# Kernel optimization log

Hardware: AMD Instinct MI355X
Metric: run time of the kernel (lower is better)

Reference implementation:

```python
import jax, jax.numpy as jnp
import numpy as np

N_LIG, N_TGT, E = 100000, 4000, 150000
D_LIG, D_TGT, H = 4, 1280, 128


def _seg_mean(feat, idx, n):
    # segment mean; isolated nodes get 0 (PyG mean aggr semantics)
    s = jax.ops.segment_sum(feat, idx, num_segments=n)
    c = jax.ops.segment_sum(jnp.ones((idx.shape[0], 1), feat.dtype), idx, num_segments=n)
    return s / jnp.maximum(c, 1.0)


def setup_inputs() -> dict:
    key = jax.random.key(0)
    ks = jax.random.split(key, 20)
    s = 0.05  # weight scale
    inp = {
        'x_ligand': jax.random.normal(ks[0], (N_LIG, D_LIG), jnp.float32),
        'x_target': jax.random.normal(ks[1], (N_TGT, D_TGT), jnp.float32),
        'edge_index': jnp.stack([
            jax.random.randint(ks[2], (E,), 0, N_LIG, jnp.int32),
            jax.random.randint(ks[3], (E,), 0, N_TGT, jnp.int32),
        ]),
        'W1lt_l': jax.random.normal(ks[4], (D_LIG, H), jnp.float32) * s,
        'b1lt':   jax.random.normal(ks[5], (H,), jnp.float32) * s,
        'W1lt_r': jax.random.normal(ks[6], (D_TGT, H), jnp.float32) * s,
        'W1tl_l': jax.random.normal(ks[7], (D_TGT, H), jnp.float32) * s,
        'b1tl':   jax.random.normal(ks[8], (H,), jnp.float32) * s,
        'W1tl_r': jax.random.normal(ks[9], (D_LIG, H), jnp.float32) * s,
        'W2lt_l': jax.random.normal(ks[10], (H, H), jnp.float32) * s,
        'b2lt':   jax.random.normal(ks[11], (H,), jnp.float32) * s,
        'W2lt_r': jax.random.normal(ks[12], (H, H), jnp.float32) * s,
        'W2tl_l': jax.random.normal(ks[13], (H, H), jnp.float32) * s,
        'b2tl':   jax.random.normal(ks[14], (H,), jnp.float32) * s,
        'W2tl_r': jax.random.normal(ks[15], (H, H), jnp.float32) * s,
        'Wp':     jax.random.normal(ks[16], (2 * H, 1), jnp.float32) * s,
        'bp':     jax.random.normal(ks[17], (1,), jnp.float32) * s,
    }
    return inp


def reference(x_ligand, x_target, edge_index,
              W1lt_l, b1lt, W1lt_r, W1tl_l, b1tl, W1tl_r,
              W2lt_l, b2lt, W2lt_r, W2tl_l, b2tl, W2tl_r, Wp, bp):
    src, dst = edge_index[0], edge_index[1]  # ligand idx, target idx

    # conv1: SAGEConv  out = lin_l(mean_j x_src[j]) + lin_r(x_dst)
    m_t = _seg_mean(x_ligand[src], dst, N_TGT)              # [N_TGT, D_LIG]
    h_t = m_t @ W1lt_l + b1lt + x_target @ W1lt_r           # [N_TGT, H]
    m_l = _seg_mean(x_target[dst], src, N_LIG)              # [N_LIG, D_TGT]
    h_l = m_l @ W1tl_l + b1tl + x_ligand @ W1tl_r           # [N_LIG, H]
    h_t = jax.nn.relu(h_t)
    h_l = jax.nn.relu(h_l)

    # conv2 (hidden -> hidden), same edge structure
    m_t2 = _seg_mean(h_l[src], dst, N_TGT)
    h_t2 = jax.nn.relu(m_t2 @ W2lt_l + b2lt + h_t @ W2lt_r)
    m_l2 = _seg_mean(h_t[dst], src, N_LIG)
    h_l2 = jax.nn.relu(m_l2 @ W2tl_l + b2tl + h_l @ W2tl_r)

    # edge predictor: gather-cat-linear
    edge_feats = jnp.concatenate([h_l2[src], h_t2[dst]], axis=-1)  # [E, 2H]
    out = (edge_feats @ Wp + bp).squeeze(-1)                        # [E]
    return out
```

## Files before the change

### kernel.cpp

```cpp
#include <hip/hip_runtime.h>
#include <hip/hip_bf16.h>

#define N_LIG 100000
#define N_TGT 4000
#define NEDGE 150000
#define DT 1280
#define HD 128
#define CAP_L 32
#define CAP_T 128
#define NTILE_L 6250
#define NTILE_PAD 6252
#define PL_BLOCKS 1563

typedef __attribute__((ext_vector_type(8))) short short8v;
typedef __attribute__((ext_vector_type(4))) float f32x4;

static __device__ __forceinline__ ushort f2bf(float f) {
    __hip_bfloat16 h = __float2bfloat16(f);
    union { __hip_bfloat16 h; ushort u; } c; c.h = h; return c.u;
}
static __device__ __forceinline__ float bf2f(ushort u) {
    union { unsigned v; float f; } c; c.v = ((unsigned)u) << 16; return c.f;
}

__global__ __launch_bounds__(256) void k_pack(
    const float* __restrict__ W2, uint4* __restrict__ Wf,
    const float* __restrict__ Wr, const float* __restrict__ Wl,
    uint4* __restrict__ Wf1,
    const float* __restrict__ xt, uint4* __restrict__ xtf,
    int4* __restrict__ cntz,
    const float* __restrict__ W2a, const float* __restrict__ W2b,
    uint4* __restrict__ Wf2)
{
    int bx = blockIdx.x;
    if (bx < 8) {
        int gid = bx * 256 + threadIdx.x;
        int lane = gid & 63, frag = gid >> 6;
        int ks = frag >> 3, ct = frag & 7;
        int l15 = lane & 15, g = lane >> 4;
        int k = ks * 32 + g * 4, n = ct * 16 + l15;
        union { ushort us[8]; uint4 u; } o;
#pragma unroll
        for (int j = 0; j < 4; ++j) {
            o.us[j]     = f2bf(W2[(size_t)(k + j) * HD + n]);
            o.us[4 + j] = f2bf(W2[(size_t)(k + 16 + j) * HD + n]);
        }
        Wf[gid] = o.u;
    } else if (bx < 168) {
        int gid = (bx - 8) * 256 + threadIdx.x;
        int lane = gid & 63, frag = gid >> 6;
        int ks = frag >> 4, nct = frag & 15;
        int l15 = lane & 15, g = lane >> 4;
        int k = ks * 32 + g * 4, n = nct * 16 + l15;
        const float* Ws = (n < HD) ? Wr : Wl;
        int nn = n & 127;
        union { ushort us[8]; uint4 u; } o;
#pragma unroll
        for (int j = 0; j < 4; ++j) {
            o.us[j]     = f2bf(Ws[(size_t)(k + j) * HD + nn]);
            o.us[4 + j] = f2bf(Ws[(size_t)(k + 16 + j) * HD + nn]);
        }
        Wf1[gid] = o.u;
    } else if (bx < 2668) {
        int gid = (bx - 168) * 256 + threadIdx.x;
        int lane = gid & 63, frag = gid >> 6;
        int ks = frag % 40, rt = frag / 40;
        int row = rt * 16 + (lane & 15);
        int kb = ks * 32 + (lane >> 4) * 4;
        float4 a0 = *reinterpret_cast<const float4*>(xt + (size_t)row * DT + kb);
        float4 a1 = *reinterpret_cast<const float4*>(xt + (size_t)row * DT + kb + 16);
        union { ushort us[8]; uint4 u; } o;
        o.us[0] = f2bf(a0.x); o.us[1] = f2bf(a0.y); o.us[2] = f2bf(a0.z); o.us[3] = f2bf(a0.w);
        o.us[4] = f2bf(a1.x); o.us[5] = f2bf(a1.y); o.us[6] = f2bf(a1.z); o.us[7] = f2bf(a1.w);
        xtf[gid] = o.u;
    } else if (bx < 2770) {
        int i = (bx - 2668) * 256 + threadIdx.x;
        if (i < 26000) cntz[i] = make_int4(0, 0, 0, 0);
    } else {
        int gid = (bx - 2770) * 256 + threadIdx.x;
        int lane = gid & 63, frag = gid >> 6;
        int ks = frag >> 4, nct = frag & 15;
        int l15 = lane & 15, g = lane >> 4;
        int k = ks * 32 + g * 4, n = nct * 16 + l15;
        const float* Ws = (n < HD) ? W2a : W2b;
        int nn = n & 127;
        union { ushort us[8]; uint4 u; } o;
#pragma unroll
        for (int j = 0; j < 4; ++j) {
            o.us[j]     = f2bf(Ws[(size_t)(k + j) * HD + nn]);
            o.us[4 + j] = f2bf(Ws[(size_t)(k + 16 + j) * HD + nn]);
        }
        Wf2[gid] = o.u;
    }
}

__global__ __launch_bounds__(256) void k_fill(
    const int* __restrict__ src, const int* __restrict__ dst,
    int* __restrict__ cnt_src, int* __restrict__ cnt_dst,
    int* __restrict__ bsrc, int* __restrict__ bdst)
{
    int e = blockIdx.x * 256 + threadIdx.x;
    if (e >= NEDGE) return;
    int s = src[e], d = dst[e];
    int ps = atomicAdd(&cnt_src[s], 1);
    if (ps < CAP_L) bsrc[(size_t)s * CAP_L + ps] = d;
    int pd = atomicAdd(&cnt_dst[d], 1);
    if (pd < CAP_T) bdst[(size_t)d * CAP_T + pd] = s;
}

__global__ __launch_bounds__(512) void k_tgt1m(
    const uint4* __restrict__ xtf,
    const uint4* __restrict__ Wf1,
    const uint4* __restrict__ Wf2,
    const float* __restrict__ xl,
    const int* __restrict__ bdst, const int* __restrict__ cnt_dst,
    const float* __restrict__ W1lt_l,
    const float* __restrict__ b1lt,
    float* __restrict__ y_t1,
    float* __restrict__ y_t2, float* __restrict__ htW2r)
{
    __shared__ float  ms[16][4];
    __shared__ ushort hts[16][136];

    int w = threadIdx.x >> 6;
    int lane = threadIdx.x & 63;
    int l15 = lane & 15, g = lane >> 4;
    int rt = blockIdx.x;
    int row0 = rt * 16;

    if (threadIdx.x < 128) {
        int r = threadIdx.x >> 3, lane8 = threadIdx.x & 7;
        int row = row0 + r;
        int deg = cnt_dst[row];
        int n = min(deg, CAP_T);
        float4 acc = make_float4(0.f, 0.f, 0.f, 0.f);
        for (int i = lane8; i < n; i += 8) {
            int sid = bdst[(size_t)row * CAP_T + i];
            float4 x = *reinterpret_cast<const float4*>(xl + 4ull * (unsigned)sid);
            acc.x += x.x; acc.y += x.y; acc.z += x.z; acc.w += x.w;
        }
#pragma unroll
        for (int off = 1; off < 8; off <<= 1) {
            acc.x += __shfl_xor(acc.x, off); acc.y += __shfl_xor(acc.y, off);
            acc.z += __shfl_xor(acc.z, off); acc.w += __shfl_xor(acc.w, off);
        }
        if (lane8 == 0) {
            float dinv = 1.0f / fmaxf((float)deg, 1.0f);
            ms[r][0] = acc.x * dinv; ms[r][1] = acc.y * dinv;
            ms[r][2] = acc.z * dinv; ms[r][3] = acc.w * dinv;
        }
    }

    f32x4 acc[2];
#pragma unroll
    for (int ct = 0; ct < 2; ++ct) acc[ct] = (f32x4){0.f, 0.f, 0.f, 0.f};

    for (int ks = 0; ks < DT / 32; ++ks) {
        union { uint4 u; short8v s; } ua;
        ua.u = xtf[(size_t)(rt * 40 + ks) * 64 + lane];
#pragma unroll
        for (int ct = 0; ct < 2; ++ct) {
            union { uint4 u; short8v s; } ub;
            ub.u = Wf1[(size_t)(ks * 16 + w * 2 + ct) * 64 + lane];
            acc[ct] = __builtin_amdgcn_mfma_f32_16x16x32_bf16(ua.s, ub.s, acc[ct], 0, 0, 0);
        }
    }

    __syncthreads();

    if (w < 4) {
#pragma unroll
        for (int ct = 0; ct < 2; ++ct) {
            int c = w * 32 + ct * 16 + l15;
            float wl0 = W1lt_l[c], wl1 = W1lt_l[HD + c],
                  wl2 = W1lt_l[2 * HD + c], wl3 = W1lt_l[3 * HD + c];
            float bb = b1lt[c];
#pragma unroll
            for (int j = 0; j < 4; ++j) {
                int r = 4 * g + j;
                float v = acc[ct][j] + bb + ms[r][0] * wl0 + ms[r][1] * wl1
                        + ms[r][2] * wl2 + ms[r][3] * wl3;
                hts[r][c] = f2bf(fmaxf(v, 0.0f));
            }
        }
    } else {
#pragma unroll
        for (int ct = 0; ct < 2; ++ct) {
            int c = (w - 4) * 32 + ct * 16 + l15;
#pragma unroll
            for (int j = 0; j < 4; ++j) {
                int grow = row0 + 4 * g + j;
                y_t1[(size_t)grow * HD + c] = acc[ct][j];
            }
        }
    }
    __syncthreads();

    f32x4 acc2[2];
#pragma unroll
    for (int ct = 0; ct < 2; ++ct) acc2[ct] = (f32x4){0.f, 0.f, 0.f, 0.f};

#pragma unroll
    for (int ks2 = 0; ks2 < 4; ++ks2) {
        int kb2 = ks2 * 32 + g * 4;
        union { ushort us[8]; short8v s; } ua2;
        *reinterpret_cast<ushort4*>(&ua2.us[0]) =
            *reinterpret_cast<const ushort4*>(&hts[l15][kb2]);
        *reinterpret_cast<ushort4*>(&ua2.us[4]) =
            *reinterpret_cast<const ushort4*>(&hts[l15][kb2 + 16]);
#pragma unroll
        for (int ct = 0; ct < 2; ++ct) {
            union { uint4 u; short8v s; } ub2;
            ub2.u = Wf2[(size_t)(ks2 * 16 + w * 2 + ct) * 64 + lane];
            acc2[ct] = __builtin_amdgcn_mfma_f32_16x16x32_bf16(ua2.s, ub2.s, acc2[ct], 0, 0, 0);
        }
    }

    float* outp = (w < 4) ? y_t2 : htW2r;
    int cw = (w < 4) ? w : (w - 4);
#pragma unroll
    for (int ct = 0; ct < 2; ++ct) {
        int c = cw * 32 + ct * 16 + l15;
#pragma unroll
        for (int j = 0; j < 4; ++j) {
            int grow = row0 + 4 * g + j;
            outp[(size_t)grow * HD + c] = acc2[ct][j];
        }
    }
}

__global__ __launch_bounds__(256) void k_hl(
    const float* __restrict__ xl,
    const float* __restrict__ y_t1, const float* __restrict__ y_t2,
    const int* __restrict__ bsrc, const int* __restrict__ cnt_src,
    const float* __restrict__ W1tl_r,
    const float* __restrict__ b1tl,
    ushort* __restrict__ hlb, uint4* __restrict__ hlbf,
    ushort* __restrict__ gl2)
{
    int tc = threadIdx.x & 15;
    int node = blockIdx.x * 16 + (threadIdx.x >> 4);
    int ks = tc >> 2, g = tc & 3;
    int kb = ks * 32 + g * 4;

    int deg = cnt_src[node];
    int n = min(deg, CAP_L);
    float4 s0 = make_float4(0.f, 0.f, 0.f, 0.f);
    float4 s1 = make_float4(0.f, 0.f, 0.f, 0.f);
    float4 t0 = make_float4(0.f, 0.f, 0.f, 0.f);
    float4 t1 = make_float4(0.f, 0.f, 0.f, 0.f);
    for (int i = 0; i < n; ++i) {
        int did = bsrc[(size_t)node * CAP_L + i];
        float4 v0 = *reinterpret_cast<const float4*>(y_t1 + (size_t)did * HD + kb);
        float4 v1 = *reinterpret_cast<const float4*>(y_t1 + (size_t)did * HD + kb + 16);
        float4 u0 = *reinterpret_cast<const float4*>(y_t2 + (size_t)did * HD + kb);
        float4 u1 = *reinterpret_cast<const float4*>(y_t2 + (size_t)did * HD + kb + 16);
        s0.x += v0.x; s0.y += v0.y; s0.z += v0.z; s0.w += v0.w;
        s1.x += v1.x; s1.y += v1.y; s1.z += v1.z; s1.w += v1.w;
        t0.x += u0.x; t0.y += u0.y; t0.z += u0.z; t0.w += u0.w;
        t1.x += u1.x; t1.y += u1.y; t1.z += u1.z; t1.w += u1.w;
    }
    float dinv = 1.0f / fmaxf((float)deg, 1.0f);
    float4 x = *reinterpret_cast<const float4*>(xl + 4ull * (unsigned)node);

    float4 b0 = *reinterpret_cast<const float4*>(b1tl + kb);
    float4 b1 = *reinterpret_cast<const float4*>(b1tl + kb + 16);
    float4 wa0 = *reinterpret_cast<const float4*>(W1tl_r + 0 * HD + kb);
    float4 wa1 = *reinterpret_cast<const float4*>(W1tl_r + 1 * HD + kb);
    float4 wa2 = *reinterpret_cast<const float4*>(W1tl_r + 2 * HD + kb);
    float4 wa3 = *reinterpret_cast<const float4*>(W1tl_r + 3 * HD + kb);
    float4 wb0 = *reinterpret_cast<const float4*>(W1tl_r + 0 * HD + kb + 16);
    float4 wb1 = *reinterpret_cast<const float4*>(W1tl_r + 1 * HD + kb + 16);
    float4 wb2 = *reinterpret_cast<const float4*>(W1tl_r + 2 * HD + kb + 16);
    float4 wb3 = *reinterpret_cast<const float4*>(W1tl_r + 3 * HD + kb + 16);

    union { ushort us[8]; uint4 u; ushort4 h[2]; } o;
    o.us[0] = f2bf(fmaxf(s0.x * dinv + b0.x + x.x * wa0.x + x.y * wa1.x + x.z * wa2.x + x.w * wa3.x, 0.f));
    o.us[1] = f2bf(fmaxf(s0.y * dinv + b0.y + x.x * wa0.y + x.y * wa1.y + x.z * wa2.y + x.w * wa3.y, 0.f));
    o.us[2] = f2bf(fmaxf(s0.z * dinv + b0.z + x.x * wa0.z + x.y * wa1.z + x.z * wa2.z + x.w * wa3.z, 0.f));
    o.us[3] = f2bf(fmaxf(s0.w * dinv + b0.w + x.x * wa0.w + x.y * wa1.w + x.z * wa2.w + x.w * wa3.w, 0.f));
    o.us[4] = f2bf(fmaxf(s1.x * dinv + b1.x + x.x * wb0.x + x.y * wb1.x + x.z * wb2.x + x.w * wb3.x, 0.f));
    o.us[5] = f2bf(fmaxf(s1.y * dinv + b1.y + x.x * wb0.y + x.y * wb1.y + x.z * wb2.y + x.w * wb3.y, 0.f));
    o.us[6] = f2bf(fmaxf(s1.z * dinv + b1.z + x.x * wb0.z + x.y * wb1.z + x.z * wb2.z + x.w * wb3.z, 0.f));
    o.us[7] = f2bf(fmaxf(s1.w * dinv + b1.w + x.x * wb0.w + x.y * wb1.w + x.z * wb2.w + x.w * wb3.w, 0.f));

    *reinterpret_cast<ushort4*>(hlb + (size_t)node * HD + kb)      = o.h[0];
    *reinterpret_cast<ushort4*>(hlb + (size_t)node * HD + kb + 16) = o.h[1];
    int lane = (node & 15) + 16 * g;
    hlbf[(size_t)(blockIdx.x * 4 + ks) * 64 + lane] = o.u;

    ushort4 q0, q1;
    q0.x = f2bf(t0.x * dinv); q0.y = f2bf(t0.y * dinv);
    q0.z = f2bf(t0.z * dinv); q0.w = f2bf(t0.w * dinv);
    q1.x = f2bf(t1.x * dinv); q1.y = f2bf(t1.y * dinv);
    q1.z = f2bf(t1.z * dinv); q1.w = f2bf(t1.w * dinv);
    *reinterpret_cast<ushort4*>(gl2 + (size_t)node * HD + kb)      = q0;
    *reinterpret_cast<ushort4*>(gl2 + (size_t)node * HD + kb + 16) = q1;
}

__global__ __launch_bounds__(256) void k_ptl(
    const ushort* __restrict__ hlb,
    const uint4* __restrict__ hlbf,
    const uint4* __restrict__ Wf,
    const ushort* __restrict__ gl2,
    const int* __restrict__ bdst, const int* __restrict__ cnt_dst,
    const float* __restrict__ Wlt,
    const float* __restrict__ b2lt,
    const float* __restrict__ b2tl,
    const float* __restrict__ htW2r,
    const float* __restrict__ Wp,
    float* __restrict__ p_t, float* __restrict__ p_l)
{
    __shared__ int   idx[CAP_T];
    __shared__ float sm[16][132];
    __shared__ float msh[HD];
    __shared__ float sum2[2];

    if (blockIdx.x < N_TGT) {
        int row = blockIdx.x;
        int deg = cnt_dst[row];
        int nn = min(deg, CAP_T);

        if (threadIdx.x < CAP_T) idx[threadIdx.x] = bdst[(size_t)row * CAP_T + threadIdx.x];
        __syncthreads();

        int wg = threadIdx.x >> 4, l16 = threadIdx.x & 15;
        float s[8];
#pragma unroll
        for (int j = 0; j < 8; ++j) s[j] = 0.f;
        for (int i = wg; i < nn; i += 16) {
            int sid = idx[i];
            union { uint4 u; ushort us[8]; } v;
            v.u = *reinterpret_cast<const uint4*>(hlb + (size_t)sid * HD + l16 * 8);
#pragma unroll
            for (int j = 0; j < 8; ++j) s[j] += bf2f(v.us[j]);
        }
#pragma unroll
        for (int j = 0; j < 8; ++j) sm[wg][l16 * 8 + j] = s[j];
        __syncthreads();

        if (threadIdx.x < HD) {
            int h = threadIdx.x;
            float dinv = 1.0f / fmaxf((float)deg, 1.0f);
            float acc = 0.f;
#pragma unroll
            for (int w2 = 0; w2 < 16; ++w2) acc += sm[w2][h];
            msh[h] = acc * dinv;
        }
        __syncthreads();

        if (threadIdx.x < HD) {
            int h = threadIdx.x;
            float g = 0.f;
            for (int k = 0; k < HD; k += 4) {
                float4 mk = *reinterpret_cast<const float4*>(&msh[k]);
                g += mk.x * Wlt[(size_t)(k + 0) * HD + h] + mk.y * Wlt[(size_t)(k + 1) * HD + h]
                   + mk.z * Wlt[(size_t)(k + 2) * HD + h] + mk.w * Wlt[(size_t)(k + 3) * HD + h];
            }
            float v = fmaxf(g + b2lt[h] + htW2r[(size_t)row * HD + h], 0.0f);
            float part = v * Wp[HD + h];
#pragma unroll
            for (int off = 1; off < 64; off <<= 1) part += __shfl_xor(part, off);
            if ((h & 63) == 0) sum2[h >> 6] = part;
        }
        __syncthreads();
        if (threadIdx.x == 0) p_t[row] = sum2[0] + sum2[1];
        return;
    }

    int wid = threadIdx.x >> 6;
    int lane = threadIdx.x & 63;
    int l15 = lane & 15, g = lane >> 4;
    int tile = (blockIdx.x - N_TGT) * 4 + wid;
    int wrow0 = tile * 16;

    f32x4 acc[8];
#pragma unroll
    for (int ct = 0; ct < 8; ++ct) acc[ct] = (f32x4){0.f, 0.f, 0.f, 0.f};

#pragma unroll
    for (int ks = 0; ks < 4; ++ks) {
        union { uint4 u; short8v s; } ua;
        ua.u = hlbf[(size_t)(tile * 4 + ks) * 64 + lane];
#pragma unroll
        for (int ct = 0; ct < 8; ++ct) {
            union { uint4 u; short8v s; } ub;
            ub.u = Wf[(ks * 8 + ct) * 64 + lane];
            acc[ct] = __builtin_amdgcn_mfma_f32_16x16x32_bf16(ua.s, ub.s, acc[ct], 0, 0, 0);
        }
    }

    float wpv[8], bv[8];
#pragma unroll
    for (int ct = 0; ct < 8; ++ct) {
        int c = ct * 16 + l15;
        wpv[ct] = Wp[c];
        bv[ct]  = b2tl[c];
    }

#pragma unroll
    for (int j = 0; j < 4; ++j) {
        int row = wrow0 + g * 4 + j;
        bool valid = row < N_LIG;
        int lrow = valid ? row : 0;
        const ushort* gp = gl2 + (size_t)lrow * HD + l15;
        float part = 0.f;
#pragma unroll
        for (int ct = 0; ct < 8; ++ct) {
            float v = acc[ct][j] + bf2f(gp[ct * 16]) + bv[ct];
            part += fmaxf(v, 0.f) * wpv[ct];
        }
#pragma unroll
        for (int off = 1; off < 16; off <<= 1) part += __shfl_xor(part, off);
        if (valid && l15 == 0) p_l[row] = part;
    }
}

__global__ __launch_bounds__(256) void k_out(
    const int* __restrict__ src, const int* __restrict__ dst,
    const float* __restrict__ p_l, const float* __restrict__ p_t,
    const float* __restrict__ bp, float* __restrict__ out)
{
    int e = blockIdx.x * 256 + threadIdx.x;
    if (e >= NEDGE) return;
    out[e] = p_l[src[e]] + p_t[dst[e]] + bp[0];
}

extern "C" void kernel_launch(void* const* d_in, const int* in_sizes, int n_in,
                              void* d_out, int out_size, void* d_ws, size_t ws_size,
                              hipStream_t stream)
{
    const float* x_l    = (const float*)d_in[0];
    const float* x_t    = (const float*)d_in[1];
    const int*   ei     = (const int*)  d_in[2];
    const float* W1lt_l = (const float*)d_in[3];
    const float* b1lt   = (const float*)d_in[4];
    const float* W1lt_r = (const float*)d_in[5];
    const float* W1tl_l = (const float*)d_in[6];
    const float* b1tl   = (const float*)d_in[7];
    const float* W1tl_r = (const float*)d_in[8];
    const float* W2lt_l = (const float*)d_in[9];
    const float* b2lt   = (const float*)d_in[10];
    const float* W2lt_r = (const float*)d_in[11];
    const float* W2tl_l = (const float*)d_in[12];
    const float* b2tl   = (const float*)d_in[13];
    const float* W2tl_r = (const float*)d_in[14];
    const float* Wp     = (const float*)d_in[15];
    const float* bp     = (const float*)d_in[16];

    const int* src = ei;
    const int* dst = ei + NEDGE;

    char* ws = (char*)d_ws;
    size_t o = 0;
    int* cnt_src = (int*)(ws + o); o += (size_t)N_LIG * 4;
    int* cnt_dst = (int*)(ws + o); o += (size_t)N_TGT * 4;
    int* bsrc = (int*)(ws + o); o += (size_t)N_LIG * CAP_L * 4;
    int* bdst = (int*)(ws + o); o += (size_t)N_TGT * CAP_T * 4;
    ushort* hlb  = (ushort*)(ws + o); o += (size_t)N_LIG * HD * 2;
    ushort* gl2  = (ushort*)(ws + o); o += (size_t)N_LIG * HD * 2;
    uint4* hlbf  = (uint4*)(ws + o);  o += (size_t)NTILE_PAD * 4 * 64 * 16;
    uint4* Wf    = (uint4*)(ws + o);  o += (size_t)32 * 64 * 16;
    uint4* Wf1   = (uint4*)(ws + o);  o += (size_t)640 * 64 * 16;
    uint4* Wf2   = (uint4*)(ws + o);  o += (size_t)64 * 64 * 16;
    uint4* xtf   = (uint4*)(ws + o);  o += (size_t)10000 * 64 * 16;
    float* y_t1  = (float*)(ws + o); o += (size_t)N_TGT * HD * 4;
    float* y_t2  = (float*)(ws + o); o += (size_t)N_TGT * HD * 4;
    float* htW2r = (float*)(ws + o); o += (size_t)N_TGT * HD * 4;
    float* p_l   = (float*)(ws + o); o += (size_t)N_LIG * 4;
    float* p_t   = (float*)(ws + o); o += (size_t)N_TGT * 4;

    float* out = (float*)d_out;

    k_pack<<<2786, 256, 0, stream>>>(W2tl_r, Wf, W1lt_r, W1tl_l, Wf1,
                                     x_t, xtf, (int4*)cnt_src,
                                     W2tl_l, W2lt_r, Wf2);

    k_fill<<<(NEDGE + 255) / 256, 256, 0, stream>>>(src, dst, cnt_src, cnt_dst, bsrc, bdst);

    k_tgt1m<<<N_TGT / 16, 512, 0, stream>>>(xtf, Wf1, Wf2, x_l, bdst, cnt_dst,
                                            W1lt_l, b1lt, y_t1, y_t2, htW2r);

    k_hl<<<NTILE_L, 256, 0, stream>>>(x_l, y_t1, y_t2, bsrc, cnt_src,
                                      W1tl_r, b1tl, hlb, hlbf, gl2);

    k_ptl<<<N_TGT + PL_BLOCKS, 256, 0, stream>>>(hlb, hlbf, Wf, gl2,
                                                 bdst, cnt_dst,
                                                 W2lt_l, b2lt, b2tl, htW2r, Wp,
                                                 p_t, p_l);

    k_out<<<(NEDGE + 255) / 256, 256, 0, stream>>>(src, dst, p_l, p_t, bp, out);
}
```

Measured before the change: 111.4 us.

## Split k_hl gather across two half-warps and store bf16 rows as permuted uint4

k_hl now gives each ligand node 32 threads instead of 16. One half gathers y_t1 to build h_l, and the other half gathers y_t2 to build the gl2 mean, so each thread carries half the gather work and twice as many blocks launch. The row buffers hlb and gl2 are now written as a single 16-byte store per thread in a permuted column order instead of two 8-byte stores. k_ptl is changed to read this permuted layout through remapped column indices. The trade-off is more threads doing duplicate index loads and a branch that diverges at half-warp granularity.

```diff
diff --git a/kernel.cpp b/kernel.cpp
--- a/kernel.cpp
+++ b/kernel.cpp
@@ -235,71 +235,69 @@
     const int* __restrict__ bsrc, const int* __restrict__ cnt_src,
     const float* __restrict__ W1tl_r,
     const float* __restrict__ b1tl,
-    ushort* __restrict__ hlb, uint4* __restrict__ hlbf,
-    ushort* __restrict__ gl2)
-{
-    int tc = threadIdx.x & 15;
-    int node = blockIdx.x * 16 + (threadIdx.x >> 4);
+    uint4* __restrict__ hlb,
+    uint4* __restrict__ hlbf,
+    uint4* __restrict__ gl2)
+{
+    int tc32 = threadIdx.x & 31;
+    int node = blockIdx.x * 8 + (threadIdx.x >> 5);
+    int part = tc32 >> 4;
+    int tc = tc32 & 15;
     int ks = tc >> 2, g = tc & 3;
     int kb = ks * 32 + g * 4;
 
     int deg = cnt_src[node];
     int n = min(deg, CAP_L);
+    const float* ysrc = part ? y_t2 : y_t1;
+
     float4 s0 = make_float4(0.f, 0.f, 0.f, 0.f);
     float4 s1 = make_float4(0.f, 0.f, 0.f, 0.f);
-    float4 t0 = make_float4(0.f, 0.f, 0.f, 0.f);
-    float4 t1 = make_float4(0.f, 0.f, 0.f, 0.f);
     for (int i = 0; i < n; ++i) {
         int did = bsrc[(size_t)node * CAP_L + i];
-        float4 v0 = *reinterpret_cast<const float4*>(y_t1 + (size_t)did * HD + kb);
-        float4 v1 = *reinterpret_cast<const float4*>(y_t1 + (size_t)did * HD + kb + 16);
-        float4 u0 = *reinterpret_cast<const float4*>(y_t2 + (size_t)did * HD + kb);
-        float4 u1 = *reinterpret_cast<const float4*>(y_t2 + (size_t)did * HD + kb + 16);
+        float4 v0 = *reinterpret_cast<const float4*>(ysrc + (size_t)did * HD + kb);
+        float4 v1 = *reinterpret_cast<const float4*>(ysrc + (size_t)did * HD + kb + 16);
         s0.x += v0.x; s0.y += v0.y; s0.z += v0.z; s0.w += v0.w;
         s1.x += v1.x; s1.y += v1.y; s1.z += v1.z; s1.w += v1.w;
-        t0.x += u0.x; t0.y += u0.y; t0.z += u0.z; t0.w += u0.w;
-        t1.x += u1.x; t1.y += u1.y; t1.z += u1.z; t1.w += u1.w;
     }
     float dinv = 1.0f / fmaxf((float)deg, 1.0f);
-    float4 x = *reinterpret_cast<const float4*>(xl + 4ull * (unsigned)node);
-
-    float4 b0 = *reinterpret_cast<const float4*>(b1tl + kb);
-    float4 b1 = *reinterpret_cast<const float4*>(b1tl + kb + 16);
-    float4 wa0 = *reinterpret_cast<const float4*>(W1tl_r + 0 * HD + kb);
-    float4 wa1 = *reinterpret_cast<const float4*>(W1tl_r + 1 * HD + kb);
-    float4 wa2 = *reinterpret_cast<const float4*>(W1tl_r + 2 * HD + kb);
-    float4 wa3 = *reinterpret_cast<const float4*>(W1tl_r + 3 * HD + kb);
-    float4 wb0 = *reinterpret_cast<const float4*>(W1tl_r + 0 * HD + kb + 16);
-    float4 wb1 = *reinterpret_cast<const float4*>(W1tl_r + 1 * HD + kb + 16);
-    float4 wb2 = *reinterpret_cast<const float4*>(W1tl_r + 2 * HD + kb + 16);
-    float4 wb3 = *reinterpret_cast<const float4*>(W1tl_r + 3 * HD + kb + 16);
-
-    union { ushort us[8]; uint4 u; ushort4 h[2]; } o;
-    o.us[0] = f2bf(fmaxf(s0.x * dinv + b0.x + x.x * wa0.x + x.y * wa1.x + x.z * wa2.x + x.w * wa3.x, 0.f));
-    o.us[1] = f2bf(fmaxf(s0.y * dinv + b0.y + x.x * wa0.y + x.y * wa1.y + x.z * wa2.y + x.w * wa3.y, 0.f));
-    o.us[2] = f2bf(fmaxf(s0.z * dinv + b0.z + x.x * wa0.z + x.y * wa1.z + x.z * wa2.z + x.w * wa3.z, 0.f));
-    o.us[3] = f2bf(fmaxf(s0.w * dinv + b0.w + x.x * wa0.w + x.y * wa1.w + x.z * wa2.w + x.w * wa3.w, 0.f));
-    o.us[4] = f2bf(fmaxf(s1.x * dinv + b1.x + x.x * wb0.x + x.y * wb1.x + x.z * wb2.x + x.w * wb3.x, 0.f));
-    o.us[5] = f2bf(fmaxf(s1.y * dinv + b1.y + x.x * wb0.y + x.y * wb1.y + x.z * wb2.y + x.w * wb3.y, 0.f));
-    o.us[6] = f2bf(fmaxf(s1.z * dinv + b1.z + x.x * wb0.z + x.y * wb1.z + x.z * wb2.z + x.w * wb3.z, 0.f));
-    o.us[7] = f2bf(fmaxf(s1.w * dinv + b1.w + x.x * wb0.w + x.y * wb1.w + x.z * wb2.w + x.w * wb3.w, 0.f));
-
-    *reinterpret_cast<ushort4*>(hlb + (size_t)node * HD + kb)      = o.h[0];
-    *reinterpret_cast<ushort4*>(hlb + (size_t)node * HD + kb + 16) = o.h[1];
-    int lane = (node & 15) + 16 * g;
-    hlbf[(size_t)(blockIdx.x * 4 + ks) * 64 + lane] = o.u;
-
-    ushort4 q0, q1;
-    q0.x = f2bf(t0.x * dinv); q0.y = f2bf(t0.y * dinv);
-    q0.z = f2bf(t0.z * dinv); q0.w = f2bf(t0.w * dinv);
-    q1.x = f2bf(t1.x * dinv); q1.y = f2bf(t1.y * dinv);
-    q1.z = f2bf(t1.z * dinv); q1.w = f2bf(t1.w * dinv);
-    *reinterpret_cast<ushort4*>(gl2 + (size_t)node * HD + kb)      = q0;
-    *reinterpret_cast<ushort4*>(gl2 + (size_t)node * HD + kb + 16) = q1;
+
+    union { ushort us[8]; uint4 u; } o;
+    if (part == 0) {
+        float4 x = *reinterpret_cast<const float4*>(xl + 4ull * (unsigned)node);
+        float4 b0 = *reinterpret_cast<const float4*>(b1tl + kb);
+        float4 b1 = *reinterpret_cast<const float4*>(b1tl + kb + 16);
+        float4 wa0 = *reinterpret_cast<const float4*>(W1tl_r + 0 * HD + kb);
+        float4 wa1 = *reinterpret_cast<const float4*>(W1tl_r + 1 * HD + kb);
+        float4 wa2 = *reinterpret_cast<const float4*>(W1tl_r + 2 * HD + kb);
+        float4 wa3 = *reinterpret_cast<const float4*>(W1tl_r + 3 * HD + kb);
+        float4 wb0 = *reinterpret_cast<const float4*>(W1tl_r + 0 * HD + kb + 16);
+        float4 wb1 = *reinterpret_cast<const float4*>(W1tl_r + 1 * HD + kb + 16);
+        float4 wb2 = *reinterpret_cast<const float4*>(W1tl_r + 2 * HD + kb + 16);
+        float4 wb3 = *reinterpret_cast<const float4*>(W1tl_r + 3 * HD + kb + 16);
+
+        o.us[0] = f2bf(fmaxf(s0.x * dinv + b0.x + x.x * wa0.x + x.y * wa1.x + x.z * wa2.x + x.w * wa3.x, 0.f));
+        o.us[1] = f2bf(fmaxf(s0.y * dinv + b0.y + x.x * wa0.y + x.y * wa1.y + x.z * wa2.y + x.w * wa3.y, 0.f));
+        o.us[2] = f2bf(fmaxf(s0.z * dinv + b0.z + x.x * wa0.z + x.y * wa1.z + x.z * wa2.z + x.w * wa3.z, 0.f));
+        o.us[3] = f2bf(fmaxf(s0.w * dinv + b0.w + x.x * wa0.w + x.y * wa1.w + x.z * wa2.w + x.w * wa3.w, 0.f));
+        o.us[4] = f2bf(fmaxf(s1.x * dinv + b1.x + x.x * wb0.x + x.y * wb1.x + x.z * wb2.x + x.w * wb3.x, 0.f));
+        o.us[5] = f2bf(fmaxf(s1.y * dinv + b1.y + x.x * wb0.y + x.y * wb1.y + x.z * wb2.y + x.w * wb3.y, 0.f));
+        o.us[6] = f2bf(fmaxf(s1.z * dinv + b1.z + x.x * wb0.z + x.y * wb1.z + x.z * wb2.z + x.w * wb3.z, 0.f));
+        o.us[7] = f2bf(fmaxf(s1.w * dinv + b1.w + x.x * wb0.w + x.y * wb1.w + x.z * wb2.w + x.w * wb3.w, 0.f));
+
+        hlb[(size_t)node * 16 + tc] = o.u;
+        int lane = (node & 15) + 16 * g;
+        hlbf[(size_t)((node >> 4) * 4 + ks) * 64 + lane] = o.u;
+    } else {
+        o.us[0] = f2bf(s0.x * dinv); o.us[1] = f2bf(s0.y * dinv);
+        o.us[2] = f2bf(s0.z * dinv); o.us[3] = f2bf(s0.w * dinv);
+        o.us[4] = f2bf(s1.x * dinv); o.us[5] = f2bf(s1.y * dinv);
+        o.us[6] = f2bf(s1.z * dinv); o.us[7] = f2bf(s1.w * dinv);
+        gl2[(size_t)node * 16 + tc] = o.u;
+    }
 }
 
 __global__ __launch_bounds__(256) void k_ptl(
-    const ushort* __restrict__ hlb,
+    const uint4* __restrict__ hlb,
     const uint4* __restrict__ hlbf,
     const uint4* __restrict__ Wf,
     const ushort* __restrict__ gl2,
@@ -331,7 +329,7 @@
         for (int i = wg; i < nn; i += 16) {
             int sid = idx[i];
             union { uint4 u; ushort us[8]; } v;
-            v.u = *reinterpret_cast<const uint4*>(hlb + (size_t)sid * HD + l16 * 8);
+            v.u = hlb[(size_t)sid * 16 + l16];
 #pragma unroll
             for (int j = 0; j < 8; ++j) s[j] += bf2f(v.us[j]);
         }
@@ -341,11 +339,14 @@
 
         if (threadIdx.x < HD) {
             int h = threadIdx.x;
+            int tc2 = h >> 3, jj = h & 7;
             float dinv = 1.0f / fmaxf((float)deg, 1.0f);
             float acc = 0.f;
 #pragma unroll
-            for (int w2 = 0; w2 < 16; ++w2) acc += sm[w2][h];
-            msh[h] = acc * dinv;
+            for (int w2 = 0; w2 < 16; ++w2) acc += sm[w2][tc2 * 8 + jj];
+            int ks2 = tc2 >> 2, g2 = tc2 & 3;
+            int col = ks2 * 32 + ((jj >> 2) << 4) + g2 * 4 + (jj & 3);
+            msh[col] = acc * dinv;
         }
         __syncthreads();
 
@@ -391,11 +392,13 @@
     }
 
     float wpv[8], bv[8];
+    int off8[8];
 #pragma unroll
     for (int ct = 0; ct < 8; ++ct) {
         int c = ct * 16 + l15;
         wpv[ct] = Wp[c];
         bv[ct]  = b2tl[c];
+        off8[ct] = (((ct >> 1) * 4 + (l15 >> 2)) << 3) + ((ct & 1) << 2) + (l15 & 3);
     }
 
 #pragma unroll
@@ -403,11 +406,11 @@
         int row = wrow0 + g * 4 + j;
         bool valid = row < N_LIG;
         int lrow = valid ? row : 0;
-        const ushort* gp = gl2 + (size_t)lrow * HD + l15;
+        const ushort* gp = gl2 + (size_t)lrow * HD;
         float part = 0.f;
 #pragma unroll
         for (int ct = 0; ct < 8; ++ct) {
-            float v = acc[ct][j] + bf2f(gp[ct * 16]) + bv[ct];
+            float v = acc[ct][j] + bf2f(gp[off8[ct]]) + bv[ct];
             part += fmaxf(v, 0.f) * wpv[ct];
         }
 #pragma unroll
@@ -457,8 +460,8 @@
     int* cnt_dst = (int*)(ws + o); o += (size_t)N_TGT * 4;
     int* bsrc = (int*)(ws + o); o += (size_t)N_LIG * CAP_L * 4;
     int* bdst = (int*)(ws + o); o += (size_t)N_TGT * CAP_T * 4;
-    ushort* hlb  = (ushort*)(ws + o); o += (size_t)N_LIG * HD * 2;
-    ushort* gl2  = (ushort*)(ws + o); o += (size_t)N_LIG * HD * 2;
+    uint4* hlb   = (uint4*)(ws + o);  o += (size_t)N_LIG * HD * 2;
+    uint4* gl2   = (uint4*)(ws + o);  o += (size_t)N_LIG * HD * 2;
     uint4* hlbf  = (uint4*)(ws + o);  o += (size_t)NTILE_PAD * 4 * 64 * 16;
     uint4* Wf    = (uint4*)(ws + o);  o += (size_t)32 * 64 * 16;
     uint4* Wf1   = (uint4*)(ws + o);  o += (size_t)640 * 64 * 16;
@@ -481,10 +484,10 @@
     k_tgt1m<<<N_TGT / 16, 512, 0, stream>>>(xtf, Wf1, Wf2, x_l, bdst, cnt_dst,
                                             W1lt_l, b1lt, y_t1, y_t2, htW2r);
 
-    k_hl<<<NTILE_L, 256, 0, stream>>>(x_l, y_t1, y_t2, bsrc, cnt_src,
-                                      W1tl_r, b1tl, hlb, hlbf, gl2);
-
-    k_ptl<<<N_TGT + PL_BLOCKS, 256, 0, stream>>>(hlb, hlbf, Wf, gl2,
+    k_hl<<<N_LIG / 8, 256, 0, stream>>>(x_l, y_t1, y_t2, bsrc, cnt_src,
+                                        W1tl_r, b1tl, hlb, hlbf, gl2);
+
+    k_ptl<<<N_TGT + PL_BLOCKS, 256, 0, stream>>>(hlb, hlbf, Wf, (const ushort*)gl2,
                                                  bdst, cnt_dst,
                                                  W2lt_l, b2lt, b2tl, htW2r, Wp,
                                                  p_t, p_l);
```

Measured after the change: 131.5 us. 18.0% more time.
